# Kernel tuning notes

Measured on AMD Instinct MI355X. Metric: run time of the kernel, lower is better.

## Reference

```python
import jax, jax.numpy as jnp
import numpy as np

N, C, H, M = 4096, 1024, 16, 4096
D = C // H
EPS = 1e-6


def rms_norm(x, g):
    # RMSNorm32: normalize in fp32 with eps=1e-6, affine scale g
    x32 = x.astype(jnp.float32)
    inv = jax.lax.rsqrt(jnp.mean(x32 * x32, axis=-1, keepdims=True) + EPS)
    return (x32 * inv).astype(x.dtype) * g


def setup_inputs() -> dict:
    key = jax.random.key(0)
    ks = jax.random.split(key, 6)
    s = 1.0 / np.sqrt(C)
    return {
        "x": jax.random.normal(ks[0], (N, C), jnp.float32),
        "g1": jnp.ones((C,), jnp.float32),
        "g2": jnp.ones((C,), jnp.float32),
        "w_qkv": jax.random.normal(ks[1], (C, 3 * C), jnp.float32) * s,
        "w_o": jax.random.normal(ks[2], (C, C), jnp.float32) * s,
        "w1": jax.random.normal(ks[3], (C, M), jnp.float32) * s,
        "w2": jax.random.normal(ks[4], (M, C), jnp.float32) * (1.0 / np.sqrt(M)),
    }


def reference(x, g1, g2, w_qkv, w_o, w1, w2):
    # --- pre-norm + full multi-head self-attention over all N sparse tokens ---
    h = rms_norm(x, g1)                                   # [N, C]
    qkv = (h @ w_qkv).reshape(N, 3, H, D)                 # [N, 3, H, D]
    q, k, v = qkv[:, 0], qkv[:, 1], qkv[:, 2]             # [N, H, D]
    scale = 1.0 / np.sqrt(D)
    scores = jnp.einsum('nhd,mhd->hnm', q, k) * scale     # [H, N, N]
    attn = jax.nn.softmax(scores, axis=-1)
    o = jnp.einsum('hnm,mhd->nhd', attn, v).reshape(N, C) # [N, C]
    x = x + o @ w_o                                       # residual
    # --- pre-norm + gated-free MLP (GELU tanh) ---
    h2 = rms_norm(x, g2)
    m = jax.nn.gelu(h2 @ w1, approximate=True) @ w2       # [N, C]
    return x + m
```

## Files before the change

### kernel.cpp

```cpp
#include <hip/hip_runtime.h>
#include <stdint.h>

#define TOK 4096
#define CH  1024
#define NH  16
#define HD  64
#define FF  4096

typedef __attribute__((ext_vector_type(8))) short bf16x8;
typedef __attribute__((ext_vector_type(4))) float f32x4;
typedef __attribute__((ext_vector_type(16))) float f32x16;

__device__ __forceinline__ unsigned short f2bf(float f) {
    union { float f; unsigned u; } v; v.f = f;
    unsigned u = v.u;
    u += 0x7fffu + ((u >> 16) & 1u);
    return (unsigned short)(u >> 16);
}

__device__ __forceinline__ unsigned cvtpk(float a, float b) {
    unsigned r;
    asm("v_cvt_pk_bf16_f32 %0, %1, %2" : "=v"(r) : "v"(a), "v"(b));
    return r;
}

__device__ __forceinline__ void load_lds16(const void* g, void* l) {
    __builtin_amdgcn_global_load_lds(
        (const __attribute__((address_space(1))) unsigned int*)g,
        (__attribute__((address_space(3))) unsigned int*)l, 16, 0, 0);
}

template<int N> __device__ __forceinline__ void wait_vm_lgkm0() {
    if constexpr (N == 0)      asm volatile("s_waitcnt vmcnt(0) lgkmcnt(0)" ::: "memory");
    else if constexpr (N == 3) asm volatile("s_waitcnt vmcnt(3) lgkmcnt(0)" ::: "memory");
    else if constexpr (N == 4) asm volatile("s_waitcnt vmcnt(4) lgkmcnt(0)" ::: "memory");
    __builtin_amdgcn_sched_barrier(0);
    __builtin_amdgcn_s_barrier();
}

__device__ __forceinline__ float gelu_tanh(float u) {
    float z = 0.7978845608028654f * (u + 0.044715f * u * u * u);
    float e = __expf(2.0f * z);
    return 0.5f * u * (1.0f + (1.0f - 2.0f / (e + 1.0f)));
}

__global__ __launch_bounds__(256) void wT_kernel(const float* __restrict__ in,
                                                 unsigned short* __restrict__ out,
                                                 int K, int Nn) {
    __shared__ float tile[32][33];
    int k0 = blockIdx.x * 32, n0 = blockIdx.y * 32;
    int t = threadIdx.x, r = t >> 3, c = t & 7;
#pragma unroll
    for (int i = 0; i < 4; i++)
        tile[r][c + 8 * i] = in[(size_t)(k0 + r) * Nn + n0 + c + 8 * i];
    __syncthreads();
#pragma unroll
    for (int i = 0; i < 4; i++)
        out[(size_t)(n0 + r) * K + k0 + c + 8 * i] = f2bf(tile[c + 8 * i][r]);
}

__global__ __launch_bounds__(256) void rms_kernel(const float* __restrict__ x,
                                                  const float* __restrict__ g,
                                                  unsigned short* __restrict__ out) {
    int row = blockIdx.x, t = threadIdx.x;
    const float4* xr = (const float4*)(x + (size_t)row * CH);
    float4 v = xr[t];
    float ss = v.x * v.x + v.y * v.y + v.z * v.z + v.w * v.w;
#pragma unroll
    for (int m = 32; m; m >>= 1) ss += __shfl_xor(ss, m, 64);
    __shared__ float wsum[4];
    if ((t & 63) == 0) wsum[t >> 6] = ss;
    __syncthreads();
    float inv = rsqrtf((wsum[0] + wsum[1] + wsum[2] + wsum[3]) * (1.0f / CH) + 1e-6f);
    float4 gv = ((const float4*)g)[t];
    ushort4 o;
    o.x = f2bf(v.x * inv * gv.x);
    o.y = f2bf(v.y * inv * gv.y);
    o.z = f2bf(v.z * inv * gv.z);
    o.w = f2bf(v.w * inv * gv.w);
    ((ushort4*)(out + (size_t)row * CH))[t] = o;
}

template<int BM, int BN, int EPI>
__global__ __launch_bounds__(256) void gemm_bt(const unsigned short* __restrict__ A,
                                               const unsigned short* __restrict__ Bt,
                                               void* __restrict__ outp,
                                               const float* __restrict__ resid,
                                               int M, int Nn, int K) {
    __shared__ __align__(16) unsigned short ldsA[3][BM * 32];
    __shared__ __align__(16) unsigned short ldsB[3][BN * 32];
    constexpr int LPS = BM / 64 + BN / 64;
    const int t = threadIdx.x, l = t & 63, w = t >> 6;
    const int nbn = Nn / BN;
    const int bid = blockIdx.x, nwg = gridDim.x, cpx = nwg >> 3;
    const int swz = (bid & 7) * cpx + (bid >> 3);
    const int bm = swz / nbn, bn = swz % nbn;
    const int wr = w >> 1, wc = w & 1;
    constexpr int MF = BM / 32, NF = BN / 32;
    const unsigned short* Ag = A + (size_t)bm * BM * K;
    const unsigned short* Bg = Bt + (size_t)bn * BN * K;

    f32x4 acc[MF][NF];
#pragma unroll
    for (int m = 0; m < MF; m++)
#pragma unroll
        for (int n = 0; n < NF; n++) acc[m][n] = {0.f, 0.f, 0.f, 0.f};

    auto stage = [&](int buf, int kt) {
#pragma unroll
        for (int p = 0; p < BM / 64; p++) {
            int c = t + 256 * p;
            load_lds16(Ag + (size_t)(c >> 2) * K + kt * 32 + (c & 3) * 8, &ldsA[buf][c * 8]);
        }
#pragma unroll
        for (int p = 0; p < BN / 64; p++) {
            int c = t + 256 * p;
            load_lds16(Bg + (size_t)(c >> 2) * K + kt * 32 + (c & 3) * 8, &ldsB[buf][c * 8]);
        }
    };

    const int nkt = K >> 5;
    stage(0, 0);
    stage(1, 1);
    wait_vm_lgkm0<LPS>();

    for (int kt = 0; kt < nkt; kt++) {
        const int buf = kt % 3;
        if (kt + 2 < nkt) stage((kt + 2) % 3, kt + 2);
        bf16x8 af[MF], bfr[NF];
#pragma unroll
        for (int m = 0; m < MF; m++)
            af[m] = *(const bf16x8*)&ldsA[buf][(wr * (BM / 2) + m * 16 + (l & 15)) * 32 + (l >> 4) * 8];
#pragma unroll
        for (int n = 0; n < NF; n++)
            bfr[n] = *(const bf16x8*)&ldsB[buf][(wc * (BN / 2) + n * 16 + (l & 15)) * 32 + (l >> 4) * 8];
#pragma unroll
        for (int m = 0; m < MF; m++)
#pragma unroll
            for (int n = 0; n < NF; n++)
                acc[m][n] = __builtin_amdgcn_mfma_f32_16x16x32_bf16(af[m], bfr[n], acc[m][n], 0, 0, 0);
        if (kt + 1 < nkt) {
            if (kt + 2 < nkt) wait_vm_lgkm0<LPS>();
            else              wait_vm_lgkm0<0>();
        }
    }

    const int r0 = bm * BM + wr * (BM / 2), c0 = bn * BN + wc * (BN / 2);
#pragma unroll
    for (int m = 0; m < MF; m++)
#pragma unroll
        for (int n = 0; n < NF; n++)
#pragma unroll
            for (int r = 0; r < 4; r++) {
                int rr = r0 + m * 16 + (l >> 4) * 4 + r;
                int cc = c0 + n * 16 + (l & 15);
                float v = acc[m][n][r];
                if (EPI == 0) {
                    ((unsigned short*)outp)[(size_t)rr * Nn + cc] = f2bf(v);
                } else if (EPI == 1) {
                    ((unsigned short*)outp)[(size_t)rr * Nn + cc] = f2bf(gelu_tanh(v));
                } else if (EPI == 3) {
                    float sc = (cc < 1024) ? 0.180336880f : 1.0f;
                    ((unsigned short*)outp)[(size_t)rr * Nn + cc] = f2bf(v * sc);
                } else {
                    ((float*)outp)[(size_t)rr * Nn + cc] = resid[(size_t)rr * Nn + cc] + v;
                }
            }
}

__global__ __launch_bounds__(256) void vT_kernel(const unsigned short* __restrict__ qkv,
                                                 unsigned short* __restrict__ vT) {
    __shared__ unsigned short tile[64][80];
    const int t = threadIdx.x;
    const int t0 = blockIdx.x * 64;
    const int h = blockIdx.y;
#pragma unroll
    for (int p = 0; p < 2; p++) {
        int c = t + 256 * p;
        int r = c >> 3, c8 = (c & 7) * 8;
        bf16x8 v = *(const bf16x8*)(qkv + (size_t)(t0 + r) * 3072 + 2048 + h * 64 + c8);
        *(bf16x8*)&tile[r][c8] = v;
    }
    __syncthreads();
#pragma unroll
    for (int p = 0; p < 2; p++) {
        int c = t + 256 * p;
        int col = c >> 3, r8 = (c & 7) * 8;
        union { unsigned short u[8]; bf16x8 v; } o;
#pragma unroll
        for (int j = 0; j < 8; j++) o.u[j] = tile[r8 + j][col];
        *(bf16x8*)(vT + (size_t)(h * 64 + col) * 4096 + t0 + r8) = o.v;
    }
}

__global__ __launch_bounds__(256) void attn_kernel(const unsigned short* __restrict__ qkv,
                                                   const unsigned short* __restrict__ vT,
                                                   unsigned short* __restrict__ o) {
    __shared__ __align__(16) unsigned short Kl[3][4096];
    __shared__ __align__(16) unsigned short Vl[3][4096];
    const int t = threadIdx.x, l = t & 63, w = t >> 6;
    const int h = blockIdx.y;
    const int qrow = blockIdx.x * 128 + w * 32 + (l & 31);

    bf16x8 qf[4];
    {
        const unsigned short* qp = qkv + (size_t)qrow * 3072 + h * 64 + ((l >> 5) * 8);
#pragma unroll
        for (int c = 0; c < 4; c++) qf[c] = *(const bf16x8*)(qp + 16 * c);
    }
    const unsigned short* kb = qkv + 1024 + h * 64;
    const unsigned short* vb = vT + (size_t)h * 64 * 4096;

    int off8[4];
#pragma unroll
    for (int c = 0; c < 4; c++)
        off8[c] = (l & 31) * 64 + ((((l >> 5) + 2 * c) ^ (l & 7)) * 8);
    int kst[2], vst[2];
#pragma unroll
    for (int p = 0; p < 2; p++) {
        int c = t + 256 * p;
        int r = c >> 3, b = c & 7;
        kst[p] = r * 3072 + ((b ^ (r & 7)) * 8);
        vst[p] = r * 4096 + ((b ^ (r & 7)) * 8);
    }

    float lrun = 0.f;
    const f32x16 z16 = {0.f, 0.f, 0.f, 0.f, 0.f, 0.f, 0.f, 0.f,
                        0.f, 0.f, 0.f, 0.f, 0.f, 0.f, 0.f, 0.f};
    f32x16 accO[2];
#pragma unroll
    for (int dt = 0; dt < 2; dt++) accO[dt] = z16;

    auto stage = [&](int buf, int kt) {
#pragma unroll
        for (int p = 0; p < 2; p++)
            load_lds16(kb + (size_t)kt * 64 * 3072 + kst[p], &Kl[buf][(t + 256 * p) * 8]);
#pragma unroll
        for (int p = 0; p < 2; p++)
            load_lds16(vb + kt * 64 + vst[p], &Vl[buf][(t + 256 * p) * 8]);
    };

    stage(0, 0);
    stage(1, 1);
    wait_vm_lgkm0<4>();

    for (int kt = 0; kt < 64; kt++) {
        const int cur = kt % 3;
        if (kt + 2 < 64) stage((kt + 2) % 3, kt + 2);

        f32x16 s[2];
        __builtin_amdgcn_s_setprio(1);
#pragma unroll
        for (int st = 0; st < 2; st++) {
            bf16x8 kf0 = *(const bf16x8*)&Kl[cur][st * 2048 + off8[0]];
            s[st] = __builtin_amdgcn_mfma_f32_32x32x16_bf16(kf0, qf[0], z16, 0, 0, 0);
#pragma unroll
            for (int c = 1; c < 4; c++) {
                bf16x8 kf = *(const bf16x8*)&Kl[cur][st * 2048 + off8[c]];
                s[st] = __builtin_amdgcn_mfma_f32_32x32x16_bf16(kf, qf[c], s[st], 0, 0, 0);
            }
        }
        __builtin_amdgcn_s_setprio(0);

        float rs = 0.f;
#pragma unroll
        for (int st = 0; st < 2; st++)
#pragma unroll
            for (int i = 0; i < 16; i++) {
                float p = __builtin_amdgcn_exp2f(s[st][i]);
                s[st][i] = p;
                rs += p;
            }
        lrun += rs;

#pragma unroll
        for (int kc = 0; kc < 4; kc++) {
            const int base = 8 * (kc & 1);
            const f32x16& S = s[kc >> 1];
            unsigned w0 = cvtpk(S[base + 0], S[base + 1]);
            unsigned w1 = cvtpk(S[base + 2], S[base + 3]);
            unsigned w2 = cvtpk(S[base + 4], S[base + 5]);
            unsigned w3 = cvtpk(S[base + 6], S[base + 7]);
            asm("v_permlane32_swap_b32 %0, %1" : "+v"(w0), "+v"(w2));
            asm("v_permlane32_swap_b32 %0, %1" : "+v"(w1), "+v"(w3));
            union { unsigned u[4]; bf16x8 v; } pf;
            pf.u[0] = w0; pf.u[1] = w1; pf.u[2] = w2; pf.u[3] = w3;
            __builtin_amdgcn_s_setprio(1);
#pragma unroll
            for (int dt = 0; dt < 2; dt++) {
                bf16x8 vf = *(const bf16x8*)&Vl[cur][dt * 2048 + off8[kc]];
                accO[dt] = __builtin_amdgcn_mfma_f32_32x32x16_bf16(vf, pf.v, accO[dt], 0, 0, 0);
            }
            __builtin_amdgcn_s_setprio(0);
        }

        if (kt < 63) {
            if (kt + 2 < 64) wait_vm_lgkm0<4>();
            else             wait_vm_lgkm0<0>();
        }
    }

    lrun += __shfl_xor(lrun, 32, 64);
    float inv = 1.0f / lrun;
    unsigned short* ob = o + (size_t)qrow * CH + h * 64 + 4 * (l >> 5);
#pragma unroll
    for (int dt = 0; dt < 2; dt++)
#pragma unroll
        for (int qd = 0; qd < 4; qd++) {
            ushort4 pk;
            pk.x = f2bf(accO[dt][qd * 4 + 0] * inv);
            pk.y = f2bf(accO[dt][qd * 4 + 1] * inv);
            pk.z = f2bf(accO[dt][qd * 4 + 2] * inv);
            pk.w = f2bf(accO[dt][qd * 4 + 3] * inv);
            *(ushort4*)(ob + dt * 32 + qd * 8) = pk;
        }
}

extern "C" void kernel_launch(void* const* d_in, const int* in_sizes, int n_in,
                              void* d_out, int out_size, void* d_ws, size_t ws_size,
                              hipStream_t stream) {
    const float* x     = (const float*)d_in[0];
    const float* g1    = (const float*)d_in[1];
    const float* g2    = (const float*)d_in[2];
    const float* w_qkv = (const float*)d_in[3];
    const float* w_o   = (const float*)d_in[4];
    const float* w1    = (const float*)d_in[5];
    const float* w2    = (const float*)d_in[6];

    char* ws = (char*)d_ws;
    unsigned short* wqkvT = (unsigned short*)(ws);
    unsigned short* woT   = (unsigned short*)(ws + 6291456);
    unsigned short* w1T   = (unsigned short*)(ws + 8388608);
    unsigned short* w2T   = (unsigned short*)(ws + 16777216);
    unsigned short* hbuf  = (unsigned short*)(ws + 25165824);
    unsigned short* qkv   = (unsigned short*)(ws + 33554432);
    unsigned short* obuf  = (unsigned short*)(ws + 58720256);
    float*          x2    = (float*)(ws + 67108864);
    unsigned short* abuf  = (unsigned short*)(ws + 83886080);
    unsigned short* vTb   = (unsigned short*)(ws + 83886080);

    dim3 b256(256);
    wT_kernel<<<dim3(CH / 32, 3 * CH / 32), b256, 0, stream>>>(w_qkv, wqkvT, CH, 3 * CH);
    wT_kernel<<<dim3(CH / 32, CH / 32),     b256, 0, stream>>>(w_o,   woT,   CH, CH);
    wT_kernel<<<dim3(CH / 32, FF / 32),     b256, 0, stream>>>(w1,    w1T,   CH, FF);
    wT_kernel<<<dim3(FF / 32, CH / 32),     b256, 0, stream>>>(w2,    w2T,   FF, CH);

    rms_kernel<<<TOK, b256, 0, stream>>>(x, g1, hbuf);
    gemm_bt<128, 128, 3><<<(TOK / 128) * (3 * CH / 128), b256, 0, stream>>>(hbuf, wqkvT, qkv, nullptr, TOK, 3 * CH, CH);
    vT_kernel<<<dim3(TOK / 64, NH), b256, 0, stream>>>(qkv, vTb);
    attn_kernel<<<dim3(TOK / 128, NH), b256, 0, stream>>>(qkv, vTb, obuf);
    gemm_bt<64, 128, 2><<<(TOK / 64) * (CH / 128), b256, 0, stream>>>(obuf, woT, x2, x, TOK, CH, CH);
    rms_kernel<<<TOK, b256, 0, stream>>>(x2, g2, hbuf);
    gemm_bt<128, 128, 1><<<(TOK / 128) * (FF / 128), b256, 0, stream>>>(hbuf, w1T, abuf, nullptr, TOK, FF, CH);
    gemm_bt<64, 128, 2><<<(TOK / 64) * (CH / 128), b256, 0, stream>>>(abuf, w2T, (float*)d_out, x2, TOK, CH, FF);
}
```

Baseline: 325.3 us.

## Fuse V transpose into QKV GEMM epilogue and simplify GEMM pipeline

Writes the V columns of the QKV projection straight into the transposed V buffer from the GEMM epilogue, dropping the separate transpose kernel. The GEMM is also changed from a three-stage LDS pipeline with counted vmcnt waits to a two-stage double buffer synchronized by __syncthreads. The residual GEMMs use 64x64 tiles for more workgroups. Removing a pass over V saves memory traffic, but the simpler pipeline may expose more load latency in every GEMM.

```diff
diff --git a/kernel.cpp b/kernel.cpp
--- a/kernel.cpp
+++ b/kernel.cpp
@@ -32,7 +32,6 @@
 
 template<int N> __device__ __forceinline__ void wait_vm_lgkm0() {
     if constexpr (N == 0)      asm volatile("s_waitcnt vmcnt(0) lgkmcnt(0)" ::: "memory");
-    else if constexpr (N == 3) asm volatile("s_waitcnt vmcnt(3) lgkmcnt(0)" ::: "memory");
     else if constexpr (N == 4) asm volatile("s_waitcnt vmcnt(4) lgkmcnt(0)" ::: "memory");
     __builtin_amdgcn_sched_barrier(0);
     __builtin_amdgcn_s_barrier();
@@ -86,10 +85,10 @@
                                                const unsigned short* __restrict__ Bt,
                                                void* __restrict__ outp,
                                                const float* __restrict__ resid,
+                                               unsigned short* __restrict__ vout,
                                                int M, int Nn, int K) {
-    __shared__ __align__(16) unsigned short ldsA[3][BM * 32];
-    __shared__ __align__(16) unsigned short ldsB[3][BN * 32];
-    constexpr int LPS = BM / 64 + BN / 64;
+    __shared__ __align__(16) unsigned short ldsA[2][BM * 32];
+    __shared__ __align__(16) unsigned short ldsB[2][BN * 32];
     const int t = threadIdx.x, l = t & 63, w = t >> 6;
     const int nbn = Nn / BN;
     const int bid = blockIdx.x, nwg = gridDim.x, cpx = nwg >> 3;
@@ -119,14 +118,12 @@
         }
     };
 
+    stage(0, 0);
+    __syncthreads();
     const int nkt = K >> 5;
-    stage(0, 0);
-    stage(1, 1);
-    wait_vm_lgkm0<LPS>();
-
     for (int kt = 0; kt < nkt; kt++) {
-        const int buf = kt % 3;
-        if (kt + 2 < nkt) stage((kt + 2) % 3, kt + 2);
+        const int buf = kt & 1;
+        if (kt + 1 < nkt) stage(buf ^ 1, kt + 1);
         bf16x8 af[MF], bfr[NF];
 #pragma unroll
         for (int m = 0; m < MF; m++)
@@ -139,58 +136,43 @@
 #pragma unroll
             for (int n = 0; n < NF; n++)
                 acc[m][n] = __builtin_amdgcn_mfma_f32_16x16x32_bf16(af[m], bfr[n], acc[m][n], 0, 0, 0);
-        if (kt + 1 < nkt) {
-            if (kt + 2 < nkt) wait_vm_lgkm0<LPS>();
-            else              wait_vm_lgkm0<0>();
-        }
+        __syncthreads();
     }
 
     const int r0 = bm * BM + wr * (BM / 2), c0 = bn * BN + wc * (BN / 2);
+    const bool vpart = (EPI == 3) && (c0 >= 2048);
 #pragma unroll
     for (int m = 0; m < MF; m++)
 #pragma unroll
-        for (int n = 0; n < NF; n++)
-#pragma unroll
-            for (int r = 0; r < 4; r++) {
-                int rr = r0 + m * 16 + (l >> 4) * 4 + r;
+        for (int n = 0; n < NF; n++) {
+            if (vpart) {
                 int cc = c0 + n * 16 + (l & 15);
-                float v = acc[m][n][r];
-                if (EPI == 0) {
-                    ((unsigned short*)outp)[(size_t)rr * Nn + cc] = f2bf(v);
-                } else if (EPI == 1) {
-                    ((unsigned short*)outp)[(size_t)rr * Nn + cc] = f2bf(gelu_tanh(v));
-                } else if (EPI == 3) {
-                    float sc = (cc < 1024) ? 0.180336880f : 1.0f;
-                    ((unsigned short*)outp)[(size_t)rr * Nn + cc] = f2bf(v * sc);
-                } else {
-                    ((float*)outp)[(size_t)rr * Nn + cc] = resid[(size_t)rr * Nn + cc] + v;
+                int rrb = r0 + m * 16 + (l >> 4) * 4;
+                ushort4 pk;
+                pk.x = f2bf(acc[m][n][0]);
+                pk.y = f2bf(acc[m][n][1]);
+                pk.z = f2bf(acc[m][n][2]);
+                pk.w = f2bf(acc[m][n][3]);
+                *(ushort4*)(vout + (size_t)(cc - 2048) * 4096 + rrb) = pk;
+            } else {
+#pragma unroll
+                for (int r = 0; r < 4; r++) {
+                    int rr = r0 + m * 16 + (l >> 4) * 4 + r;
+                    int cc = c0 + n * 16 + (l & 15);
+                    float v = acc[m][n][r];
+                    if (EPI == 0) {
+                        ((unsigned short*)outp)[(size_t)rr * Nn + cc] = f2bf(v);
+                    } else if (EPI == 1) {
+                        ((unsigned short*)outp)[(size_t)rr * Nn + cc] = f2bf(gelu_tanh(v));
+                    } else if (EPI == 3) {
+                        float sc = (cc < 1024) ? 0.180336880f : 1.0f;
+                        ((unsigned short*)outp)[(size_t)rr * Nn + cc] = f2bf(v * sc);
+                    } else {
+                        ((float*)outp)[(size_t)rr * Nn + cc] = resid[(size_t)rr * Nn + cc] + v;
+                    }
                 }
             }
-}
-
-__global__ __launch_bounds__(256) void vT_kernel(const unsigned short* __restrict__ qkv,
-                                                 unsigned short* __restrict__ vT) {
-    __shared__ unsigned short tile[64][80];
-    const int t = threadIdx.x;
-    const int t0 = blockIdx.x * 64;
-    const int h = blockIdx.y;
-#pragma unroll
-    for (int p = 0; p < 2; p++) {
-        int c = t + 256 * p;
-        int r = c >> 3, c8 = (c & 7) * 8;
-        bf16x8 v = *(const bf16x8*)(qkv + (size_t)(t0 + r) * 3072 + 2048 + h * 64 + c8);
-        *(bf16x8*)&tile[r][c8] = v;
-    }
-    __syncthreads();
-#pragma unroll
-    for (int p = 0; p < 2; p++) {
-        int c = t + 256 * p;
-        int col = c >> 3, r8 = (c & 7) * 8;
-        union { unsigned short u[8]; bf16x8 v; } o;
-#pragma unroll
-        for (int j = 0; j < 8; j++) o.u[j] = tile[r8 + j][col];
-        *(bf16x8*)(vT + (size_t)(h * 64 + col) * 4096 + t0 + r8) = o.v;
-    }
+        }
 }
 
 __global__ __launch_bounds__(256) void attn_kernel(const unsigned short* __restrict__ qkv,
@@ -346,11 +328,10 @@
     wT_kernel<<<dim3(FF / 32, CH / 32),     b256, 0, stream>>>(w2,    w2T,   FF, CH);
 
     rms_kernel<<<TOK, b256, 0, stream>>>(x, g1, hbuf);
-    gemm_bt<128, 128, 3><<<(TOK / 128) * (3 * CH / 128), b256, 0, stream>>>(hbuf, wqkvT, qkv, nullptr, TOK, 3 * CH, CH);
-    vT_kernel<<<dim3(TOK / 64, NH), b256, 0, stream>>>(qkv, vTb);
+    gemm_bt<128, 128, 3><<<(TOK / 128) * (3 * CH / 128), b256, 0, stream>>>(hbuf, wqkvT, qkv, nullptr, vTb, TOK, 3 * CH, CH);
     attn_kernel<<<dim3(TOK / 128, NH), b256, 0, stream>>>(qkv, vTb, obuf);
-    gemm_bt<64, 128, 2><<<(TOK / 64) * (CH / 128), b256, 0, stream>>>(obuf, woT, x2, x, TOK, CH, CH);
+    gemm_bt<64, 64, 2><<<(TOK / 64) * (CH / 64), b256, 0, stream>>>(obuf, woT, x2, x, nullptr, TOK, CH, CH);
     rms_kernel<<<TOK, b256, 0, stream>>>(x2, g2, hbuf);
-    gemm_bt<128, 128, 1><<<(TOK / 128) * (FF / 128), b256, 0, stream>>>(hbuf, w1T, abuf, nullptr, TOK, FF, CH);
-    gemm_bt<64, 128, 2><<<(TOK / 64) * (CH / 128), b256, 0, stream>>>(abuf, w2T, (float*)d_out, x2, TOK, CH, FF);
-}
+    gemm_bt<128, 128, 1><<<(TOK / 128) * (FF / 128), b256, 0, stream>>>(hbuf, w1T, abuf, nullptr, nullptr, TOK, FF, CH);
+    gemm_bt<64, 64, 2><<<(TOK / 64) * (CH / 64), b256, 0, stream>>>(abuf, w2T, (float*)d_out, x2, nullptr, TOK, CH, FF);
+}
```

Result: faster. 305.8 us (-6.0%).
